# Kernel optimization log

Hardware: AMD Instinct MI355X
Metric: run time of the kernel (lower is better)

Reference implementation:

```python
import jax, jax.numpy as jnp
import numpy as np

D_MODEL = 768
D_STATE = 128
EXPAND = 2
D_CONV = 4
HEADDIM = 48
D_INNER = EXPAND * D_MODEL            # 1536
NHEADS = D_INNER // HEADDIM           # 32
CONV_DIM = D_INNER + 2 * D_STATE      # 1792 (ngroups=1)
D_IN_PROJ = 2 * D_INNER + 2 * D_STATE + NHEADS  # 3360
EPS = 1e-5


def setup_inputs() -> dict:
    key = jax.random.key(0)
    ks = jax.random.split(key, 8)
    B, L = 2, 1024
    x = jax.random.normal(ks[0], (B, L, D_MODEL), dtype=jnp.float32)
    in_proj_w = jax.random.normal(ks[1], (D_IN_PROJ, D_MODEL), dtype=jnp.float32) * 0.02
    conv_w = jax.random.normal(ks[2], (CONV_DIM, D_CONV), dtype=jnp.float32) * 0.1
    conv_b = jnp.zeros((CONV_DIM,), dtype=jnp.float32)
    # dt init as in Mamba2: dt ~ logspace[1e-3, 1e-1], dt_bias = softplus^-1(dt)
    u = jax.random.uniform(ks[3], (NHEADS,), dtype=jnp.float32)
    dt = jnp.exp(u * (np.log(0.1) - np.log(0.001)) + np.log(0.001))
    dt_bias = jnp.log(jnp.expm1(dt))
    # A in [1, 16]
    A_log = jnp.log(jax.random.uniform(ks[4], (NHEADS,), dtype=jnp.float32) * 15.0 + 1.0)
    D = jnp.ones((NHEADS,), dtype=jnp.float32)
    rms_w = jnp.ones((D_INNER,), dtype=jnp.float32)
    out_proj_w = jax.random.normal(ks[5], (D_MODEL, D_INNER), dtype=jnp.float32) * 0.02
    ln_w = jnp.ones((D_MODEL,), dtype=jnp.float32)
    ln_b = jnp.zeros((D_MODEL,), dtype=jnp.float32)
    return {"x": x, "in_proj_w": in_proj_w, "conv_w": conv_w, "conv_b": conv_b,
            "dt_bias": dt_bias, "A_log": A_log, "D": D, "rms_w": rms_w,
            "out_proj_w": out_proj_w, "ln_w": ln_w, "ln_b": ln_b}


def _mamba_block(x, in_proj_w, conv_w, conv_b, dt_bias, A_log, D, rms_w, out_proj_w, ln_w, ln_b):
    B, L, _ = x.shape
    zxbcdt = jnp.einsum('bld,ed->ble', x, in_proj_w)          # (B,L,D_IN_PROJ)
    z = zxbcdt[..., :D_INNER]                                  # gate
    xBC = zxbcdt[..., D_INNER:D_INNER + CONV_DIM]              # (B,L,CONV_DIM)
    dt = jax.nn.softplus(zxbcdt[..., -NHEADS:] + dt_bias)      # (B,L,H)

    # causal depthwise conv1d (kernel 4) + SiLU
    xp = jnp.pad(xBC, ((0, 0), (D_CONV - 1, 0), (0, 0)))
    conv = conv_b
    for k in range(D_CONV):
        conv = conv + xp[:, k:k + L, :] * conv_w[:, k]
    xBC = jax.nn.silu(conv)

    xs = xBC[..., :D_INNER].reshape(B, L, NHEADS, HEADDIM)     # (B,L,H,P)
    Bm = xBC[..., D_INNER:D_INNER + D_STATE]                   # (B,L,N)
    Cm = xBC[..., D_INNER + D_STATE:]                          # (B,L,N)

    A = -jnp.exp(A_log)                                        # (H,)
    dA = jnp.exp(dt * A)                                       # (B,L,H)
    xdt = xs * dt[..., None]                                   # (B,L,H,P)

    def step(h, inp):
        dA_t, xdt_t, B_t, C_t = inp                            # (B,H),(B,H,P),(B,N),(B,N)
        h = h * dA_t[:, :, None, None] + jnp.einsum('bhp,bn->bhpn', xdt_t, B_t)
        y_t = jnp.einsum('bhpn,bn->bhp', h, C_t)
        return h, y_t

    h0 = jnp.zeros((B, NHEADS, HEADDIM, D_STATE), dtype=x.dtype)
    _, ys = jax.lax.scan(step, h0,
                         (dA.transpose(1, 0, 2), xdt.transpose(1, 0, 2, 3),
                          Bm.transpose(1, 0, 2), Cm.transpose(1, 0, 2)))
    y = ys.transpose(1, 0, 2, 3) + D[None, None, :, None] * xs  # (B,L,H,P)
    y = y.reshape(B, L, D_INNER)

    # gated RMSNorm: rmsnorm(y * silu(z)) * rms_w
    yg = y * jax.nn.silu(z)
    yg = yg * jax.lax.rsqrt(jnp.mean(yg * yg, axis=-1, keepdims=True) + EPS) * rms_w
    out = jnp.einsum('ble,de->bld', yg, out_proj_w)

    # residual + LayerNorm
    r = out + x
    mu = jnp.mean(r, axis=-1, keepdims=True)
    var = jnp.mean((r - mu) ** 2, axis=-1, keepdims=True)
    return (r - mu) * jax.lax.rsqrt(var + EPS) * ln_w + ln_b


def reference(x, in_proj_w, conv_w, conv_b, dt_bias, A_log, D, rms_w, out_proj_w, ln_w, ln_b):
    return _mamba_block(x, in_proj_w, conv_w, conv_b, dt_bias, A_log, D, rms_w,
                        out_proj_w, ln_w, ln_b)
```

## Files before the change

kernel.cpp:

```cpp
#include <hip/hip_runtime.h>
#include <math.h>

#define BDIM 2
#define LLEN 1024
#define DMODEL 768
#define DINNER 1536
#define DSTATE 128
#define NH 32
#define HD 48
#define CONVD 1792
#define DPROJ 3360
#define DPROJP 3456
#define QCH 128
#define NCH 8
#define ROWS (BDIM*LLEN)

typedef unsigned short ushort_t;
typedef __attribute__((ext_vector_type(4))) short short4v;
typedef __attribute__((ext_vector_type(8))) short short8v;
typedef __attribute__((ext_vector_type(4))) float floatx4;

#define OFF_ZX   0ull
#define OFF_XBC  (OFF_ZX  + (size_t)ROWS*DPROJP)
#define OFF_DT   (OFF_XBC + (size_t)ROWS*CONVD)
#define OFF_LA   (OFF_DT  + (size_t)ROWS*NH)
#define OFF_SC   (OFF_LA  + (size_t)ROWS*NH)
#define OFF_Y    (OFF_SC  + (size_t)BDIM*NH*NCH*HD*DSTATE)
#define OFF_PP   (OFF_Y   + (size_t)ROWS*DINNER)
#define OFF_CBT  (OFF_PP  + 1024ull)
#define OFF_CBF  (OFF_CBT + 262144ull)
#define OFF_BBF  (OFF_CBF + 131072ull)
#define OFF_BTBF (OFF_BBF + 131072ull)
#define OFF_XPT  (OFF_BTBF+ 131072ull)

__device__ __forceinline__ ushort_t f2bf(float f) {
  union { float f; unsigned int u; } v; v.f = f;
  return (ushort_t)((v.u + 0x7FFFu + ((v.u >> 16) & 1u)) >> 16);
}
__device__ __forceinline__ float bf2f(short s) {
  union { unsigned int u; float f; } v; v.u = ((unsigned int)(ushort_t)s) << 16;
  return v.f;
}

#define GLOAD_LDS16(gptr, lptr) \
  __builtin_amdgcn_global_load_lds( \
      (const __attribute__((address_space(1))) void*)(gptr), \
      (__attribute__((address_space(3))) void*)(lptr), 16, 0, 0)

__global__ __launch_bounds__(256) void convert_bf16_kernel(
    const float* __restrict__ in, ushort_t* __restrict__ out, int n8) {
  const int i = blockIdx.x * 256 + threadIdx.x;
  if (i >= n8) return;
  const float4 a = ((const float4*)in)[i * 2];
  const float4 b = ((const float4*)in)[i * 2 + 1];
  short8v o;
  o[0] = (short)f2bf(a.x); o[1] = (short)f2bf(a.y);
  o[2] = (short)f2bf(a.z); o[3] = (short)f2bf(a.w);
  o[4] = (short)f2bf(b.x); o[5] = (short)f2bf(b.y);
  o[6] = (short)f2bf(b.z); o[7] = (short)f2bf(b.w);
  *(short8v*)(out + (size_t)i * 8) = o;
}

__global__ __launch_bounds__(256) void convert_wpad_kernel(
    const float* __restrict__ w, ushort_t* __restrict__ out) {
  const int i = blockIdx.x * 256 + threadIdx.x;
  if (i >= DPROJP * (DMODEL / 8)) return;
  const int row = i / (DMODEL / 8);
  short8v o;
  if (row < DPROJ) {
    const float4 a = ((const float4*)w)[i * 2];
    const float4 b = ((const float4*)w)[i * 2 + 1];
    o[0] = (short)f2bf(a.x); o[1] = (short)f2bf(a.y);
    o[2] = (short)f2bf(a.z); o[3] = (short)f2bf(a.w);
    o[4] = (short)f2bf(b.x); o[5] = (short)f2bf(b.y);
    o[6] = (short)f2bf(b.z); o[7] = (short)f2bf(b.w);
  } else {
    for (int j = 0; j < 8; j++) o[j] = 0;
  }
  *(short8v*)(out + (size_t)i * 8) = o;
}

__global__ __launch_bounds__(256) void gemm_bf16(
    const ushort_t* __restrict__ A, const ushort_t* __restrict__ B,
    float* __restrict__ C, int M, int N, int K) {
  __shared__ __align__(16) ushort_t As[128 * 32];
  __shared__ __align__(16) ushort_t Bs[128 * 32];
  const int tid = threadIdx.x;
  const int lane = tid & 63;
  const int w = tid >> 6;
  const int wm = (w >> 1) * 64, wn = (w & 1) * 64;
  const int m0 = blockIdx.y * 128, n0 = blockIdx.x * 128;

  floatx4 acc[4][4];
#pragma unroll
  for (int i = 0; i < 4; i++)
#pragma unroll
    for (int j = 0; j < 4; j++) acc[i][j] = (floatx4){0.f, 0.f, 0.f, 0.f};

  const int srow = tid >> 2;
  const int skc = (tid & 3) * 8;
  const int kk = (lane >> 4) * 8;
  const int fr = lane & 15;

  for (int k0 = 0; k0 < K; k0 += 32) {
#pragma unroll
    for (int i = 0; i < 2; i++) {
      GLOAD_LDS16(A + (size_t)(m0 + i * 64 + srow) * K + k0 + skc,
                  As + (i * 64 + srow) * 32 + skc);
      GLOAD_LDS16(B + (size_t)(n0 + i * 64 + srow) * K + k0 + skc,
                  Bs + (i * 64 + srow) * 32 + skc);
    }
    __syncthreads();
    short8v a[4], bv[4];
#pragma unroll
    for (int mr = 0; mr < 4; mr++)
      a[mr] = *(const short8v*)(As + (wm + mr * 16 + fr) * 32 + kk);
#pragma unroll
    for (int nc = 0; nc < 4; nc++)
      bv[nc] = *(const short8v*)(Bs + (wn + nc * 16 + fr) * 32 + kk);
#pragma unroll
    for (int mr = 0; mr < 4; mr++)
#pragma unroll
      for (int nc = 0; nc < 4; nc++)
        acc[mr][nc] = __builtin_amdgcn_mfma_f32_16x16x32_bf16(
            a[mr], bv[nc], acc[mr][nc], 0, 0, 0);
    __syncthreads();
  }

  const int crow = (lane >> 4) * 4;
#pragma unroll
  for (int mr = 0; mr < 4; mr++)
#pragma unroll
    for (int nc = 0; nc < 4; nc++)
#pragma unroll
      for (int j = 0; j < 4; j++)
        C[(size_t)(m0 + wm + mr * 16 + crow + j) * N + n0 + wn + nc * 16 + fr] =
            acc[mr][nc][j];
}

__global__ __launch_bounds__(256) void conv_dt_kernel(
    const float* __restrict__ zx, const float* __restrict__ conv_w,
    const float* __restrict__ conv_b, const float* __restrict__ dt_bias,
    float* __restrict__ xbc, float* __restrict__ dtbuf) {
  const int row = blockIdx.x;
  const int t = row % LLEN;
  const int tid = threadIdx.x;
  for (int c = tid; c < CONVD; c += 256) {
    float accv = conv_b[c];
#pragma unroll
    for (int k = 0; k < 4; k++) {
      const int tt = t - 3 + k;
      if (tt >= 0)
        accv += zx[(size_t)(row - 3 + k) * DPROJP + DINNER + c] * conv_w[c * 4 + k];
    }
    xbc[(size_t)row * CONVD + c] = accv / (1.f + expf(-accv));
  }
  if (tid < NH) {
    const float v = zx[(size_t)row * DPROJP + (DPROJ - NH) + tid] + dt_bias[tid];
    dtbuf[row * NH + tid] = (v > 20.f) ? v : log1pf(expf(v));
  }
}

__global__ __launch_bounds__(128) void cumsum_kernel(
    const float* __restrict__ dtb, const float* __restrict__ A_log,
    float* __restrict__ la2, float* __restrict__ Pp) {
  const int c = blockIdx.x, h = blockIdx.y, b = blockIdx.z;
  const int tid = threadIdx.x, lane = tid & 63;
  const int row = b * LLEN + c * QCH + tid;
  __shared__ float s0;
  float v = dtb[(size_t)row * NH + h];
#pragma unroll
  for (int off = 1; off < 64; off <<= 1) {
    const float u = __shfl_up(v, off, 64);
    if (lane >= off) v += u;
  }
  if (tid == 63) s0 = v;
  __syncthreads();
  if (tid >= 64) v += s0;
  const float la2v = -expf(A_log[h]) * v * 1.44269504088896f;
  la2[(size_t)row * NH + h] = la2v;
  if (tid == 127) Pp[(b * NH + h) * NCH + c] = exp2f(la2v);
}

__global__ __launch_bounds__(256) void prep_bc_kernel(
    const float* __restrict__ xbc, ushort_t* __restrict__ Bbf,
    ushort_t* __restrict__ BTbf, ushort_t* __restrict__ Cbf) {
  const int bc = blockIdx.x;
  const int b = bc / NCH, c = bc % NCH;
  const int row0 = b * LLEN + c * QCH;
  const int tid = threadIdx.x;
  __shared__ ushort_t lb[128][136];
  for (int idx = tid; idx < 128 * 32; idx += 256) {
    const int t = idx >> 5, f4 = (idx & 31) * 4;
    const float4 v = *(const float4*)&xbc[(size_t)(row0 + t) * CONVD + DINNER + f4];
    short4v o;
    o[0] = (short)f2bf(v.x); o[1] = (short)f2bf(v.y);
    o[2] = (short)f2bf(v.z); o[3] = (short)f2bf(v.w);
    *(short4v*)&Bbf[(size_t)(bc * 128 + t) * 128 + f4] = o;
    *(short4v*)&lb[t][f4] = o;
  }
  for (int idx = tid; idx < 128 * 32; idx += 256) {
    const int t = idx >> 5, f4 = (idx & 31) * 4;
    const float4 v = *(const float4*)&xbc[(size_t)(row0 + t) * CONVD + DINNER + DSTATE + f4];
    short4v o;
    o[0] = (short)f2bf(v.x); o[1] = (short)f2bf(v.y);
    o[2] = (short)f2bf(v.z); o[3] = (short)f2bf(v.w);
    *(short4v*)&Cbf[(size_t)(bc * 128 + t) * 128 + f4] = o;
  }
  __syncthreads();
  for (int idx = tid; idx < 128 * 16; idx += 256) {
    const int n = idx & 127, t0 = (idx >> 7) * 8;
    short8v o;
#pragma unroll
    for (int j = 0; j < 8; j++) o[j] = lb[t0 + j][n];
    *(short8v*)&BTbf[(size_t)(bc * 128 + n) * 128 + t0] = o;
  }
}

__global__ __launch_bounds__(256) void prep_x_kernel(
    const float* __restrict__ xbc, const float* __restrict__ dtb,
    ushort_t* __restrict__ XpT) {
  const int c = blockIdx.x, h = blockIdx.y, b = blockIdx.z;
  const int row0 = b * LLEN + c * QCH;
  const int tid = threadIdx.x;
  __shared__ ushort_t xl[128][56];
  __shared__ float dts[128];
  if (tid < 128) dts[tid] = dtb[(size_t)(row0 + tid) * NH + h];
  __syncthreads();
  for (int idx = tid; idx < 128 * 12; idx += 256) {
    const int r = idx / 12, f4 = (idx % 12) * 4;
    const float4 v = *(const float4*)&xbc[(size_t)(row0 + r) * CONVD + h * HD + f4];
    const float d = dts[r];
    short4v o;
    o[0] = (short)f2bf(v.x * d); o[1] = (short)f2bf(v.y * d);
    o[2] = (short)f2bf(v.z * d); o[3] = (short)f2bf(v.w * d);
    *(short4v*)&xl[r][f4] = o;
  }
  __syncthreads();
  const size_t base = ((size_t)(b * NCH + c) * NH + h) * HD * 128;
  for (int idx = tid; idx < 48 * 16; idx += 256) {
    const int p = idx % 48, t0 = (idx / 48) * 8;
    short8v o;
#pragma unroll
    for (int j = 0; j < 8; j++) o[j] = xl[t0 + j][p];
    *(short8v*)&XpT[base + (size_t)p * 128 + t0] = o;
  }
}

__global__ __launch_bounds__(256) void cbt_kernel(
    const ushort_t* __restrict__ Cbf, const ushort_t* __restrict__ Bbf,
    float* __restrict__ CBt) {
  const int bc = blockIdx.x;
  const int tid = threadIdx.x, lane = tid & 63, w = tid >> 6;
  const int wm = w * 32;
  const int fr = lane & 15, kk = (lane >> 4) * 8;
  floatx4 acc[2][8];
#pragma unroll
  for (int i = 0; i < 2; i++)
#pragma unroll
    for (int j = 0; j < 8; j++) acc[i][j] = (floatx4){0.f, 0.f, 0.f, 0.f};
  for (int ki = 0; ki < 4; ki++) {
    const int kg = ki * 32 + kk;
    short8v a[2], bv[8];
#pragma unroll
    for (int mt = 0; mt < 2; mt++)
      a[mt] = *(const short8v*)&Cbf[(size_t)(bc * 128 + wm + mt * 16 + fr) * 128 + kg];
#pragma unroll
    for (int nt = 0; nt < 8; nt++)
      bv[nt] = *(const short8v*)&Bbf[(size_t)(bc * 128 + nt * 16 + fr) * 128 + kg];
#pragma unroll
    for (int mt = 0; mt < 2; mt++)
#pragma unroll
      for (int nt = 0; nt < 8; nt++)
        acc[mt][nt] = __builtin_amdgcn_mfma_f32_16x16x32_bf16(
            a[mt], bv[nt], acc[mt][nt], 0, 0, 0);
  }
  const int crow = (lane >> 4) * 4;
#pragma unroll
  for (int mt = 0; mt < 2; mt++)
#pragma unroll
    for (int nt = 0; nt < 8; nt++)
#pragma unroll
      for (int j = 0; j < 4; j++)
        CBt[(size_t)(bc * 128 + wm + mt * 16 + crow + j) * 128 + nt * 16 + fr] =
            acc[mt][nt][j];
}

__global__ __launch_bounds__(256) void stateA_kernel(
    const ushort_t* __restrict__ XpT, const ushort_t* __restrict__ BTbf,
    const float* __restrict__ la2, float* __restrict__ Sc) {
  const int c = blockIdx.x, h = blockIdx.y, b = blockIdx.z;
  const int bc = b * NCH + c, bh = b * NH + h;
  const int row0 = b * LLEN + c * QCH;
  const int tid = threadIdx.x, lane = tid & 63, w = tid >> 6;
  __shared__ float ew[128];
  const float laL = la2[(size_t)(row0 + 127) * NH + h];
  if (tid < 128) ew[tid] = exp2f(laL - la2[(size_t)(row0 + tid) * NH + h]);
  __syncthreads();
  const int wn = w * 32;
  const int fr = lane & 15, kk = (lane >> 4) * 8;
  const size_t xbase = ((size_t)bc * NH + h) * HD * 128;
  floatx4 acc[3][2];
#pragma unroll
  for (int i = 0; i < 3; i++)
#pragma unroll
    for (int j = 0; j < 2; j++) acc[i][j] = (floatx4){0.f, 0.f, 0.f, 0.f};
  for (int ki = 0; ki < 4; ki++) {
    const int kg = ki * 32 + kk;
    short8v a[3], bv[2];
#pragma unroll
    for (int mt = 0; mt < 3; mt++) {
      const short8v raw = *(const short8v*)&XpT[xbase + (size_t)(mt * 16 + fr) * 128 + kg];
      short8v s;
#pragma unroll
      for (int e = 0; e < 8; e++) s[e] = (short)f2bf(bf2f(raw[e]) * ew[kg + e]);
      a[mt] = s;
    }
#pragma unroll
    for (int nt = 0; nt < 2; nt++)
      bv[nt] = *(const short8v*)&BTbf[(size_t)(bc * 128 + wn + nt * 16 + fr) * 128 + kg];
#pragma unroll
    for (int mt = 0; mt < 3; mt++)
#pragma unroll
      for (int nt = 0; nt < 2; nt++)
        acc[mt][nt] = __builtin_amdgcn_mfma_f32_16x16x32_bf16(
            a[mt], bv[nt], acc[mt][nt], 0, 0, 0);
  }
  const int crow = (lane >> 4) * 4;
  float* sc = Sc + (size_t)(bh * NCH + c) * (HD * DSTATE);
#pragma unroll
  for (int mt = 0; mt < 3; mt++)
#pragma unroll
    for (int nt = 0; nt < 2; nt++)
#pragma unroll
      for (int j = 0; j < 4; j++)
        sc[(size_t)(mt * 16 + crow + j) * 128 + wn + nt * 16 + fr] = acc[mt][nt][j];
}

__global__ __launch_bounds__(256) void chunk_combine_kernel(
    float* __restrict__ Sc, const float* __restrict__ Pp) {
  const int bh = blockIdx.x;
  const int tid = threadIdx.x;
  for (int e = tid; e < HD * DSTATE; e += 256) {
    float hv = 0.f;
#pragma unroll
    for (int c = 0; c < NCH; c++) {
      const size_t idx = ((size_t)(bh * NCH + c)) * HD * DSTATE + e;
      const float sv = Sc[idx];
      Sc[idx] = hv;
      hv = hv * Pp[bh * NCH + c] + sv;
    }
  }
}

__global__ __launch_bounds__(256) void ykernel(
    const float* __restrict__ CBt, const ushort_t* __restrict__ XpT,
    const ushort_t* __restrict__ Cbf, const float* __restrict__ Hc,
    const float* __restrict__ la2, float* __restrict__ y) {
  const int c = blockIdx.x, h = blockIdx.y, b = blockIdx.z;
  const int bc = b * NCH + c, bh = b * NH + h;
  const int row0 = b * LLEN + c * QCH;
  const int tid = threadIdx.x, lane = tid & 63, w = tid >> 6;
  __shared__ float laL[128], el[128];
  if (tid < 128) {
    const float v = la2[(size_t)(row0 + tid) * NH + h];
    laL[tid] = v; el[tid] = exp2f(v);
  }
  __syncthreads();
  const int wm = w * 32;
  const int fr = lane & 15, kk = (lane >> 4) * 8;
  const size_t xbase = ((size_t)bc * NH + h) * HD * 128;
  const float* hin = Hc + (size_t)(bh * NCH + c) * (HD * DSTATE);
  floatx4 acc[2][3];
#pragma unroll
  for (int i = 0; i < 2; i++)
#pragma unroll
    for (int j = 0; j < 3; j++) acc[i][j] = (floatx4){0.f, 0.f, 0.f, 0.f};

  for (int ki = 0; ki < 4; ki++) {
    const int kg = ki * 32 + kk;
    short8v a[2], bv[3];
#pragma unroll
    for (int mt = 0; mt < 2; mt++) {
      const int t = wm + mt * 16 + fr;
      const float lt = laL[t];
      const float* cb = &CBt[(size_t)(bc * 128 + t) * 128 + kg];
      const float4 u0 = *(const float4*)cb;
      const float4 u1 = *(const float4*)(cb + 4);
      const float f[8] = {u0.x, u0.y, u0.z, u0.w, u1.x, u1.y, u1.z, u1.w};
      short8v s;
#pragma unroll
      for (int e = 0; e < 8; e++) {
        const int sidx = kg + e;
        const float m = (t >= sidx) ? exp2f(lt - laL[sidx]) : 0.f;
        s[e] = (short)f2bf(f[e] * m);
      }
      a[mt] = s;
    }
#pragma unroll
    for (int nt = 0; nt < 3; nt++)
      bv[nt] = *(const short8v*)&XpT[xbase + (size_t)(nt * 16 + fr) * 128 + kg];
#pragma unroll
    for (int mt = 0; mt < 2; mt++)
#pragma unroll
      for (int nt = 0; nt < 3; nt++)
        acc[mt][nt] = __builtin_amdgcn_mfma_f32_16x16x32_bf16(
            a[mt], bv[nt], acc[mt][nt], 0, 0, 0);
  }
  for (int ki = 0; ki < 4; ki++) {
    const int kg = ki * 32 + kk;
    short8v a[2], bv[3];
#pragma unroll
    for (int mt = 0; mt < 2; mt++) {
      const int t = wm + mt * 16 + fr;
      const float scl = el[t];
      const short8v raw = *(const short8v*)&Cbf[(size_t)(bc * 128 + t) * 128 + kg];
      short8v s;
#pragma unroll
      for (int e = 0; e < 8; e++) s[e] = (short)f2bf(bf2f(raw[e]) * scl);
      a[mt] = s;
    }
#pragma unroll
    for (int nt = 0; nt < 3; nt++) {
      const float* hp = &hin[(size_t)(nt * 16 + fr) * 128 + kg];
      const float4 u0 = *(const float4*)hp;
      const float4 u1 = *(const float4*)(hp + 4);
      const float f[8] = {u0.x, u0.y, u0.z, u0.w, u1.x, u1.y, u1.z, u1.w};
      short8v s;
#pragma unroll
      for (int e = 0; e < 8; e++) s[e] = (short)f2bf(f[e]);
      bv[nt] = s;
    }
#pragma unroll
    for (int mt = 0; mt < 2; mt++)
#pragma unroll
      for (int nt = 0; nt < 3; nt++)
        acc[mt][nt] = __builtin_amdgcn_mfma_f32_16x16x32_bf16(
            a[mt], bv[nt], acc[mt][nt], 0, 0, 0);
  }
  const int crow = (lane >> 4) * 4;
#pragma unroll
  for (int mt = 0; mt < 2; mt++)
#pragma unroll
    for (int nt = 0; nt < 3; nt++)
#pragma unroll
      for (int j = 0; j < 4; j++) {
        const int row = row0 + wm + mt * 16 + crow + j;
        y[(size_t)row * DINNER + h * HD + nt * 16 + fr] = acc[mt][nt][j];
      }
}

__global__ __launch_bounds__(256) void gate_rms_kernel(
    const float* __restrict__ zx, const float* __restrict__ xbc,
    const float* __restrict__ Dv, const float* __restrict__ rms_w,
    const float* __restrict__ y, ushort_t* __restrict__ ybf) {
  const int row = blockIdx.x;
  const int tid = threadIdx.x;
  __shared__ float sred[4];
  float g[6];
  float ss = 0.f;
#pragma unroll
  for (int i = 0; i < 6; i++) {
    const int e = tid + i * 256;
    const float yv = y[(size_t)row * DINNER + e] + Dv[e / HD] * xbc[(size_t)row * CONVD + e];
    const float z = zx[(size_t)row * DPROJP + e];
    const float gv = yv * (z / (1.f + expf(-z)));
    g[i] = gv;
    ss += gv * gv;
  }
#pragma unroll
  for (int off = 32; off; off >>= 1) ss += __shfl_down(ss, off, 64);
  if ((tid & 63) == 0) sred[tid >> 6] = ss;
  __syncthreads();
  const float tot = sred[0] + sred[1] + sred[2] + sred[3];
  const float scale = rsqrtf(tot / DINNER + 1e-5f);
#pragma unroll
  for (int i = 0; i < 6; i++) {
    const int e = tid + i * 256;
    ybf[(size_t)row * DINNER + e] = f2bf(g[i] * scale * rms_w[e]);
  }
}

__global__ __launch_bounds__(256) void resid_ln_kernel(
    const float* __restrict__ go, const float* __restrict__ x,
    const float* __restrict__ ln_w, const float* __restrict__ ln_b,
    float* __restrict__ out) {
  const int row = blockIdx.x;
  const int tid = threadIdx.x;
  __shared__ float sred[4];
  __shared__ float sred2[4];
  float r[3];
  float s = 0.f;
#pragma unroll
  for (int i = 0; i < 3; i++) {
    const int e = tid + i * 256;
    r[i] = go[(size_t)row * DMODEL + e] + x[(size_t)row * DMODEL + e];
    s += r[i];
  }
#pragma unroll
  for (int off = 32; off; off >>= 1) s += __shfl_down(s, off, 64);
  if ((tid & 63) == 0) sred[tid >> 6] = s;
  __syncthreads();
  const float mu = (sred[0] + sred[1] + sred[2] + sred[3]) * (1.f / DMODEL);
  float s2 = 0.f;
#pragma unroll
  for (int i = 0; i < 3; i++) {
    const float d = r[i] - mu;
    s2 += d * d;
  }
#pragma unroll
  for (int off = 32; off; off >>= 1) s2 += __shfl_down(s2, off, 64);
  if ((tid & 63) == 0) sred2[tid >> 6] = s2;
  __syncthreads();
  const float var = (sred2[0] + sred2[1] + sred2[2] + sred2[3]) * (1.f / DMODEL);
  const float inv = rsqrtf(var + 1e-5f);
#pragma unroll
  for (int i = 0; i < 3; i++) {
    const int e = tid + i * 256;
    out[(size_t)row * DMODEL + e] = (r[i] - mu) * inv * ln_w[e] + ln_b[e];
  }
}

extern "C" void kernel_launch(void* const* d_in, const int* in_sizes, int n_in,
                              void* d_out, int out_size, void* d_ws, size_t ws_size,
                              hipStream_t stream) {
  const float* x          = (const float*)d_in[0];
  const float* in_proj_w  = (const float*)d_in[1];
  const float* conv_w     = (const float*)d_in[2];
  const float* conv_b     = (const float*)d_in[3];
  const float* dt_bias    = (const float*)d_in[4];
  const float* A_log      = (const float*)d_in[5];
  const float* Dv         = (const float*)d_in[6];
  const float* rms_w      = (const float*)d_in[7];
  const float* out_proj_w = (const float*)d_in[8];
  const float* ln_w       = (const float*)d_in[9];
  const float* ln_b       = (const float*)d_in[10];
  float* out = (float*)d_out;
  float* ws  = (float*)d_ws;

  float* zx   = ws + OFF_ZX;
  float* xbc  = ws + OFF_XBC;
  float* dtb  = ws + OFF_DT;
  float* la2  = ws + OFF_LA;
  float* Sc   = ws + OFF_SC;
  float* ybuf = ws + OFF_Y;
  float* Pp   = ws + OFF_PP;
  float* CBt  = ws + OFF_CBT;
  ushort_t* Cbf  = (ushort_t*)(ws + OFF_CBF);
  ushort_t* Bbf  = (ushort_t*)(ws + OFF_BBF);
  ushort_t* BTbf = (ushort_t*)(ws + OFF_BTBF);
  ushort_t* XpT  = (ushort_t*)(ws + OFF_XPT);

  ushort_t* xbf   = (ushort_t*)(ws + OFF_Y);
  ushort_t* ipwbf = (ushort_t*)(ws + OFF_Y + 786432);
  ushort_t* ybf   = (ushort_t*)(ws + OFF_SC);
  ushort_t* opwbf = (ushort_t*)(ws + OFF_SC + 1572864);
  float*    go    = ws + OFF_ZX;

  convert_bf16_kernel<<<(ROWS * DMODEL / 8 + 255) / 256, 256, 0, stream>>>(
      x, xbf, ROWS * DMODEL / 8);
  convert_wpad_kernel<<<(DPROJP * DMODEL / 8 + 255) / 256, 256, 0, stream>>>(
      in_proj_w, ipwbf);

  gemm_bf16<<<dim3(DPROJP / 128, ROWS / 128), 256, 0, stream>>>(
      xbf, ipwbf, zx, ROWS, DPROJP, DMODEL);

  conv_dt_kernel<<<ROWS, 256, 0, stream>>>(zx, conv_w, conv_b, dt_bias, xbc, dtb);

  cumsum_kernel<<<dim3(NCH, NH, BDIM), 128, 0, stream>>>(dtb, A_log, la2, Pp);
  prep_bc_kernel<<<BDIM * NCH, 256, 0, stream>>>(xbc, Bbf, BTbf, Cbf);
  prep_x_kernel<<<dim3(NCH, NH, BDIM), 256, 0, stream>>>(xbc, dtb, XpT);
  cbt_kernel<<<BDIM * NCH, 256, 0, stream>>>(Cbf, Bbf, CBt);
  stateA_kernel<<<dim3(NCH, NH, BDIM), 256, 0, stream>>>(XpT, BTbf, la2, Sc);
  chunk_combine_kernel<<<BDIM * NH, 256, 0, stream>>>(Sc, Pp);
  ykernel<<<dim3(NCH, NH, BDIM), 256, 0, stream>>>(CBt, XpT, Cbf, Sc, la2, ybuf);

  gate_rms_kernel<<<ROWS, 256, 0, stream>>>(zx, xbc, Dv, rms_w, ybuf, ybf);

  convert_bf16_kernel<<<(DMODEL * DINNER / 8 + 255) / 256, 256, 0, stream>>>(
      out_proj_w, opwbf, DMODEL * DINNER / 8);
  gemm_bf16<<<dim3(DMODEL / 128, ROWS / 128), 256, 0, stream>>>(
      ybf, opwbf, go, ROWS, DMODEL, DINNER);

  resid_ln_kernel<<<ROWS, 256, 0, stream>>>(go, x, ln_w, ln_b, out);
}
```

Baseline: 256.2 us.

## Store in-proj and conv outputs in bf16, fuse conversions, narrow out-proj tile

The in-projection GEMM now writes bf16 instead of fp32, and the conv kernel reads bf16, runs vectorized over four channels at a time, and writes xBC in bf16. The separate B/C bf16 copy buffers are dropped, so downstream kernels read directly from the bf16 xBC array. The two input conversion launches are merged into one kernel, gate_rms is vectorized to 8 elements per thread, and the out-projection GEMM uses 128x64 tiles to launch more blocks. The aim is to cut memory traffic and launch count, at the cost of extra bf16 rounding on z, dt and the conv output.

```diff
diff --git a/kernel.cpp b/kernel.cpp
--- a/kernel.cpp
+++ b/kernel.cpp
@@ -21,17 +21,15 @@
 typedef __attribute__((ext_vector_type(4))) float floatx4;
 
 #define OFF_ZX   0ull
-#define OFF_XBC  (OFF_ZX  + (size_t)ROWS*DPROJP)
-#define OFF_DT   (OFF_XBC + (size_t)ROWS*CONVD)
-#define OFF_LA   (OFF_DT  + (size_t)ROWS*NH)
-#define OFF_SC   (OFF_LA  + (size_t)ROWS*NH)
-#define OFF_Y    (OFF_SC  + (size_t)BDIM*NH*NCH*HD*DSTATE)
-#define OFF_PP   (OFF_Y   + (size_t)ROWS*DINNER)
-#define OFF_CBT  (OFF_PP  + 1024ull)
-#define OFF_CBF  (OFF_CBT + 262144ull)
-#define OFF_BBF  (OFF_CBF + 131072ull)
-#define OFF_BTBF (OFF_BBF + 131072ull)
-#define OFF_XPT  (OFF_BTBF+ 131072ull)
+#define OFF_XBC  3538944ull
+#define OFF_DT   5373952ull
+#define OFF_LA   5439488ull
+#define OFF_SC   5505024ull
+#define OFF_Y    8650752ull
+#define OFF_PP   11796480ull
+#define OFF_CBT  11797504ull
+#define OFF_BTBF 12059648ull
+#define OFF_XPT  12190720ull
 
 __device__ __forceinline__ ushort_t f2bf(float f) {
   union { float f; unsigned int u; } v; v.f = f;
@@ -46,6 +44,38 @@
   __builtin_amdgcn_global_load_lds( \
       (const __attribute__((address_space(1))) void*)(gptr), \
       (__attribute__((address_space(3))) void*)(lptr), 16, 0, 0)
+
+__global__ __launch_bounds__(256) void convert_in_kernel(
+    const float* __restrict__ x, const float* __restrict__ w,
+    ushort_t* __restrict__ xbf, ushort_t* __restrict__ ipwbf) {
+  const int blk = blockIdx.x;
+  if (blk < 768) {
+    const int i = blk * 256 + threadIdx.x;
+    const float4 a = ((const float4*)x)[i * 2];
+    const float4 b = ((const float4*)x)[i * 2 + 1];
+    short8v o;
+    o[0] = (short)f2bf(a.x); o[1] = (short)f2bf(a.y);
+    o[2] = (short)f2bf(a.z); o[3] = (short)f2bf(a.w);
+    o[4] = (short)f2bf(b.x); o[5] = (short)f2bf(b.y);
+    o[6] = (short)f2bf(b.z); o[7] = (short)f2bf(b.w);
+    *(short8v*)(xbf + (size_t)i * 8) = o;
+  } else {
+    const int i = (blk - 768) * 256 + threadIdx.x;
+    const int row = i / (DMODEL / 8);
+    short8v o;
+    if (row < DPROJ) {
+      const float4 a = ((const float4*)w)[i * 2];
+      const float4 b = ((const float4*)w)[i * 2 + 1];
+      o[0] = (short)f2bf(a.x); o[1] = (short)f2bf(a.y);
+      o[2] = (short)f2bf(a.z); o[3] = (short)f2bf(a.w);
+      o[4] = (short)f2bf(b.x); o[5] = (short)f2bf(b.y);
+      o[6] = (short)f2bf(b.z); o[7] = (short)f2bf(b.w);
+    } else {
+      for (int j = 0; j < 8; j++) o[j] = 0;
+    }
+    *(short8v*)(ipwbf + (size_t)i * 8) = o;
+  }
+}
 
 __global__ __launch_bounds__(256) void convert_bf16_kernel(
     const float* __restrict__ in, ushort_t* __restrict__ out, int n8) {
@@ -61,47 +91,21 @@
   *(short8v*)(out + (size_t)i * 8) = o;
 }
 
-__global__ __launch_bounds__(256) void convert_wpad_kernel(
-    const float* __restrict__ w, ushort_t* __restrict__ out) {
-  const int i = blockIdx.x * 256 + threadIdx.x;
-  if (i >= DPROJP * (DMODEL / 8)) return;
-  const int row = i / (DMODEL / 8);
-  short8v o;
-  if (row < DPROJ) {
-    const float4 a = ((const float4*)w)[i * 2];
-    const float4 b = ((const float4*)w)[i * 2 + 1];
-    o[0] = (short)f2bf(a.x); o[1] = (short)f2bf(a.y);
-    o[2] = (short)f2bf(a.z); o[3] = (short)f2bf(a.w);
-    o[4] = (short)f2bf(b.x); o[5] = (short)f2bf(b.y);
-    o[6] = (short)f2bf(b.z); o[7] = (short)f2bf(b.w);
-  } else {
-    for (int j = 0; j < 8; j++) o[j] = 0;
-  }
-  *(short8v*)(out + (size_t)i * 8) = o;
-}
-
-__global__ __launch_bounds__(256) void gemm_bf16(
+__global__ __launch_bounds__(256) void gemm_bf16_bfout(
     const ushort_t* __restrict__ A, const ushort_t* __restrict__ B,
-    float* __restrict__ C, int M, int N, int K) {
+    ushort_t* __restrict__ C, int M, int N, int K) {
   __shared__ __align__(16) ushort_t As[128 * 32];
   __shared__ __align__(16) ushort_t Bs[128 * 32];
-  const int tid = threadIdx.x;
-  const int lane = tid & 63;
-  const int w = tid >> 6;
+  const int tid = threadIdx.x, lane = tid & 63, w = tid >> 6;
   const int wm = (w >> 1) * 64, wn = (w & 1) * 64;
   const int m0 = blockIdx.y * 128, n0 = blockIdx.x * 128;
-
   floatx4 acc[4][4];
 #pragma unroll
   for (int i = 0; i < 4; i++)
 #pragma unroll
     for (int j = 0; j < 4; j++) acc[i][j] = (floatx4){0.f, 0.f, 0.f, 0.f};
-
-  const int srow = tid >> 2;
-  const int skc = (tid & 3) * 8;
-  const int kk = (lane >> 4) * 8;
-  const int fr = lane & 15;
-
+  const int srow = tid >> 2, skc = (tid & 3) * 8;
+  const int kk = (lane >> 4) * 8, fr = lane & 15;
   for (int k0 = 0; k0 < K; k0 += 32) {
 #pragma unroll
     for (int i = 0; i < 2; i++) {
@@ -126,12 +130,59 @@
             a[mr], bv[nc], acc[mr][nc], 0, 0, 0);
     __syncthreads();
   }
-
   const int crow = (lane >> 4) * 4;
 #pragma unroll
   for (int mr = 0; mr < 4; mr++)
 #pragma unroll
     for (int nc = 0; nc < 4; nc++)
+#pragma unroll
+      for (int j = 0; j < 4; j++)
+        C[(size_t)(m0 + wm + mr * 16 + crow + j) * N + n0 + wn + nc * 16 + fr] =
+            f2bf(acc[mr][nc][j]);
+}
+
+__global__ __launch_bounds__(256) void gemm_bf16_n64(
+    const ushort_t* __restrict__ A, const ushort_t* __restrict__ B,
+    float* __restrict__ C, int M, int N, int K) {
+  __shared__ __align__(16) ushort_t As[128 * 32];
+  __shared__ __align__(16) ushort_t Bs[64 * 32];
+  const int tid = threadIdx.x, lane = tid & 63, w = tid >> 6;
+  const int wm = (w >> 1) * 64, wn = (w & 1) * 32;
+  const int m0 = blockIdx.y * 128, n0 = blockIdx.x * 64;
+  floatx4 acc[4][2];
+#pragma unroll
+  for (int i = 0; i < 4; i++)
+#pragma unroll
+    for (int j = 0; j < 2; j++) acc[i][j] = (floatx4){0.f, 0.f, 0.f, 0.f};
+  const int srow = tid >> 2, skc = (tid & 3) * 8;
+  const int kk = (lane >> 4) * 8, fr = lane & 15;
+  for (int k0 = 0; k0 < K; k0 += 32) {
+#pragma unroll
+    for (int i = 0; i < 2; i++)
+      GLOAD_LDS16(A + (size_t)(m0 + i * 64 + srow) * K + k0 + skc,
+                  As + (i * 64 + srow) * 32 + skc);
+    GLOAD_LDS16(B + (size_t)(n0 + srow) * K + k0 + skc, Bs + srow * 32 + skc);
+    __syncthreads();
+    short8v a[4], bv[2];
+#pragma unroll
+    for (int mr = 0; mr < 4; mr++)
+      a[mr] = *(const short8v*)(As + (wm + mr * 16 + fr) * 32 + kk);
+#pragma unroll
+    for (int nc = 0; nc < 2; nc++)
+      bv[nc] = *(const short8v*)(Bs + (wn + nc * 16 + fr) * 32 + kk);
+#pragma unroll
+    for (int mr = 0; mr < 4; mr++)
+#pragma unroll
+      for (int nc = 0; nc < 2; nc++)
+        acc[mr][nc] = __builtin_amdgcn_mfma_f32_16x16x32_bf16(
+            a[mr], bv[nc], acc[mr][nc], 0, 0, 0);
+    __syncthreads();
+  }
+  const int crow = (lane >> 4) * 4;
+#pragma unroll
+  for (int mr = 0; mr < 4; mr++)
+#pragma unroll
+    for (int nc = 0; nc < 2; nc++)
 #pragma unroll
       for (int j = 0; j < 4; j++)
         C[(size_t)(m0 + wm + mr * 16 + crow + j) * N + n0 + wn + nc * 16 + fr] =
@@ -139,24 +190,38 @@
 }
 
 __global__ __launch_bounds__(256) void conv_dt_kernel(
-    const float* __restrict__ zx, const float* __restrict__ conv_w,
+    const ushort_t* __restrict__ zxb, const float* __restrict__ conv_w,
     const float* __restrict__ conv_b, const float* __restrict__ dt_bias,
-    float* __restrict__ xbc, float* __restrict__ dtbuf) {
+    ushort_t* __restrict__ xbcb, float* __restrict__ dtbuf) {
   const int row = blockIdx.x;
   const int t = row % LLEN;
   const int tid = threadIdx.x;
-  for (int c = tid; c < CONVD; c += 256) {
-    float accv = conv_b[c];
+  for (int g = tid; g < CONVD / 4; g += 256) {
+    const int c = g * 4;
+    const float4 cb = *(const float4*)&conv_b[c];
+    float acc0 = cb.x, acc1 = cb.y, acc2 = cb.z, acc3 = cb.w;
+    float4 cw[4];
+#pragma unroll
+    for (int j = 0; j < 4; j++) cw[j] = *(const float4*)&conv_w[(c + j) * 4];
 #pragma unroll
     for (int k = 0; k < 4; k++) {
-      const int tt = t - 3 + k;
-      if (tt >= 0)
-        accv += zx[(size_t)(row - 3 + k) * DPROJP + DINNER + c] * conv_w[c * 4 + k];
-    }
-    xbc[(size_t)row * CONVD + c] = accv / (1.f + expf(-accv));
+      if (t - 3 + k >= 0) {
+        const short4v v = *(const short4v*)&zxb[(size_t)(row - 3 + k) * DPROJP + DINNER + c];
+        acc0 += bf2f(v[0]) * ((const float*)&cw[0])[k];
+        acc1 += bf2f(v[1]) * ((const float*)&cw[1])[k];
+        acc2 += bf2f(v[2]) * ((const float*)&cw[2])[k];
+        acc3 += bf2f(v[3]) * ((const float*)&cw[3])[k];
+      }
+    }
+    short4v o;
+    o[0] = (short)f2bf(acc0 / (1.f + expf(-acc0)));
+    o[1] = (short)f2bf(acc1 / (1.f + expf(-acc1)));
+    o[2] = (short)f2bf(acc2 / (1.f + expf(-acc2)));
+    o[3] = (short)f2bf(acc3 / (1.f + expf(-acc3)));
+    *(short4v*)&xbcb[(size_t)row * CONVD + c] = o;
   }
   if (tid < NH) {
-    const float v = zx[(size_t)row * DPROJP + (DPROJ - NH) + tid] + dt_bias[tid];
+    const float v = bf2f(zxb[(size_t)row * DPROJP + (DPROJ - NH) + tid]) + dt_bias[tid];
     dtbuf[row * NH + tid] = (v > 20.f) ? v : log1pf(expf(v));
   }
 }
@@ -182,9 +247,8 @@
   if (tid == 127) Pp[(b * NH + h) * NCH + c] = exp2f(la2v);
 }
 
-__global__ __launch_bounds__(256) void prep_bc_kernel(
-    const float* __restrict__ xbc, ushort_t* __restrict__ Bbf,
-    ushort_t* __restrict__ BTbf, ushort_t* __restrict__ Cbf) {
+__global__ __launch_bounds__(256) void prep_bt_kernel(
+    const ushort_t* __restrict__ xbcb, ushort_t* __restrict__ BTbf) {
   const int bc = blockIdx.x;
   const int b = bc / NCH, c = bc % NCH;
   const int row0 = b * LLEN + c * QCH;
@@ -192,20 +256,8 @@
   __shared__ ushort_t lb[128][136];
   for (int idx = tid; idx < 128 * 32; idx += 256) {
     const int t = idx >> 5, f4 = (idx & 31) * 4;
-    const float4 v = *(const float4*)&xbc[(size_t)(row0 + t) * CONVD + DINNER + f4];
-    short4v o;
-    o[0] = (short)f2bf(v.x); o[1] = (short)f2bf(v.y);
-    o[2] = (short)f2bf(v.z); o[3] = (short)f2bf(v.w);
-    *(short4v*)&Bbf[(size_t)(bc * 128 + t) * 128 + f4] = o;
-    *(short4v*)&lb[t][f4] = o;
-  }
-  for (int idx = tid; idx < 128 * 32; idx += 256) {
-    const int t = idx >> 5, f4 = (idx & 31) * 4;
-    const float4 v = *(const float4*)&xbc[(size_t)(row0 + t) * CONVD + DINNER + DSTATE + f4];
-    short4v o;
-    o[0] = (short)f2bf(v.x); o[1] = (short)f2bf(v.y);
-    o[2] = (short)f2bf(v.z); o[3] = (short)f2bf(v.w);
-    *(short4v*)&Cbf[(size_t)(bc * 128 + t) * 128 + f4] = o;
+    const short4v v = *(const short4v*)&xbcb[(size_t)(row0 + t) * CONVD + DINNER + f4];
+    *(short4v*)&lb[t][f4] = v;
   }
   __syncthreads();
   for (int idx = tid; idx < 128 * 16; idx += 256) {
@@ -218,7 +270,7 @@
 }
 
 __global__ __launch_bounds__(256) void prep_x_kernel(
-    const float* __restrict__ xbc, const float* __restrict__ dtb,
+    const ushort_t* __restrict__ xbcb, const float* __restrict__ dtb,
     ushort_t* __restrict__ XpT) {
   const int c = blockIdx.x, h = blockIdx.y, b = blockIdx.z;
   const int row0 = b * LLEN + c * QCH;
@@ -229,11 +281,11 @@
   __syncthreads();
   for (int idx = tid; idx < 128 * 12; idx += 256) {
     const int r = idx / 12, f4 = (idx % 12) * 4;
-    const float4 v = *(const float4*)&xbc[(size_t)(row0 + r) * CONVD + h * HD + f4];
+    const short4v v = *(const short4v*)&xbcb[(size_t)(row0 + r) * CONVD + h * HD + f4];
     const float d = dts[r];
     short4v o;
-    o[0] = (short)f2bf(v.x * d); o[1] = (short)f2bf(v.y * d);
-    o[2] = (short)f2bf(v.z * d); o[3] = (short)f2bf(v.w * d);
+    o[0] = (short)f2bf(bf2f(v[0]) * d); o[1] = (short)f2bf(bf2f(v[1]) * d);
+    o[2] = (short)f2bf(bf2f(v[2]) * d); o[3] = (short)f2bf(bf2f(v[3]) * d);
     *(short4v*)&xl[r][f4] = o;
   }
   __syncthreads();
@@ -248,9 +300,10 @@
 }
 
 __global__ __launch_bounds__(256) void cbt_kernel(
-    const ushort_t* __restrict__ Cbf, const ushort_t* __restrict__ Bbf,
-    float* __restrict__ CBt) {
+    const ushort_t* __restrict__ xbcb, float* __restrict__ CBt) {
   const int bc = blockIdx.x;
+  const int b = bc / NCH, c = bc % NCH;
+  const int row0 = b * LLEN + c * QCH;
   const int tid = threadIdx.x, lane = tid & 63, w = tid >> 6;
   const int wm = w * 32;
   const int fr = lane & 15, kk = (lane >> 4) * 8;
@@ -264,10 +317,12 @@
     short8v a[2], bv[8];
 #pragma unroll
     for (int mt = 0; mt < 2; mt++)
-      a[mt] = *(const short8v*)&Cbf[(size_t)(bc * 128 + wm + mt * 16 + fr) * 128 + kg];
+      a[mt] = *(const short8v*)&xbcb[(size_t)(row0 + wm + mt * 16 + fr) * CONVD +
+                                     DINNER + DSTATE + kg];
 #pragma unroll
     for (int nt = 0; nt < 8; nt++)
-      bv[nt] = *(const short8v*)&Bbf[(size_t)(bc * 128 + nt * 16 + fr) * 128 + kg];
+      bv[nt] = *(const short8v*)&xbcb[(size_t)(row0 + nt * 16 + fr) * CONVD +
+                                      DINNER + kg];
 #pragma unroll
     for (int mt = 0; mt < 2; mt++)
 #pragma unroll
@@ -355,7 +410,7 @@
 
 __global__ __launch_bounds__(256) void ykernel(
     const float* __restrict__ CBt, const ushort_t* __restrict__ XpT,
-    const ushort_t* __restrict__ Cbf, const float* __restrict__ Hc,
+    const ushort_t* __restrict__ xbcb, const float* __restrict__ Hc,
     const float* __restrict__ la2, float* __restrict__ y) {
   const int c = blockIdx.x, h = blockIdx.y, b = blockIdx.z;
   const int bc = b * NCH + c, bh = b * NH + h;
@@ -414,7 +469,8 @@
     for (int mt = 0; mt < 2; mt++) {
       const int t = wm + mt * 16 + fr;
       const float scl = el[t];
-      const short8v raw = *(const short8v*)&Cbf[(size_t)(bc * 128 + t) * 128 + kg];
+      const short8v raw = *(const short8v*)&xbcb[(size_t)(row0 + t) * CONVD +
+                                                 DINNER + DSTATE + kg];
       short8v s;
 #pragma unroll
       for (int e = 0; e < 8; e++) s[e] = (short)f2bf(bf2f(raw[e]) * scl);
@@ -451,22 +507,33 @@
 }
 
 __global__ __launch_bounds__(256) void gate_rms_kernel(
-    const float* __restrict__ zx, const float* __restrict__ xbc,
+    const ushort_t* __restrict__ zxb, const ushort_t* __restrict__ xbcb,
     const float* __restrict__ Dv, const float* __restrict__ rms_w,
     const float* __restrict__ y, ushort_t* __restrict__ ybf) {
   const int row = blockIdx.x;
   const int tid = threadIdx.x;
   __shared__ float sred[4];
-  float g[6];
+  float g[8];
   float ss = 0.f;
-#pragma unroll
-  for (int i = 0; i < 6; i++) {
-    const int e = tid + i * 256;
-    const float yv = y[(size_t)row * DINNER + e] + Dv[e / HD] * xbc[(size_t)row * CONVD + e];
-    const float z = zx[(size_t)row * DPROJP + e];
-    const float gv = yv * (z / (1.f + expf(-z)));
-    g[i] = gv;
-    ss += gv * gv;
+  if (tid < 192) {
+    const int e0 = tid * 8;
+    const short8v xv = *(const short8v*)&xbcb[(size_t)row * CONVD + e0];
+    const short8v zv = *(const short8v*)&zxb[(size_t)row * DPROJP + e0];
+    const float4 y0 = *(const float4*)&y[(size_t)row * DINNER + e0];
+    const float4 y1 = *(const float4*)&y[(size_t)row * DINNER + e0 + 4];
+    const float yf[8] = {y0.x, y0.y, y0.z, y0.w, y1.x, y1.y, y1.z, y1.w};
+#pragma unroll
+    for (int j = 0; j < 8; j++) {
+      const int e = e0 + j;
+      const float yv = yf[j] + Dv[e / HD] * bf2f(xv[j]);
+      const float z = bf2f(zv[j]);
+      const float gv = yv * (z / (1.f + expf(-z)));
+      g[j] = gv;
+      ss += gv * gv;
+    }
+  } else {
+#pragma unroll
+    for (int j = 0; j < 8; j++) g[j] = 0.f;
   }
 #pragma unroll
   for (int off = 32; off; off >>= 1) ss += __shfl_down(ss, off, 64);
@@ -474,10 +541,15 @@
   __syncthreads();
   const float tot = sred[0] + sred[1] + sred[2] + sred[3];
   const float scale = rsqrtf(tot / DINNER + 1e-5f);
-#pragma unroll
-  for (int i = 0; i < 6; i++) {
-    const int e = tid + i * 256;
-    ybf[(size_t)row * DINNER + e] = f2bf(g[i] * scale * rms_w[e]);
+  if (tid < 192) {
+    const int e0 = tid * 8;
+    const float4 w0 = *(const float4*)&rms_w[e0];
+    const float4 w1 = *(const float4*)&rms_w[e0 + 4];
+    const float wf[8] = {w0.x, w0.y, w0.z, w0.w, w1.x, w1.y, w1.z, w1.w};
+    short8v o;
+#pragma unroll
+    for (int j = 0; j < 8; j++) o[j] = (short)f2bf(g[j] * scale * wf[j]);
+    *(short8v*)&ybf[(size_t)row * DINNER + e0] = o;
   }
 }
 
@@ -538,16 +610,14 @@
   float* out = (float*)d_out;
   float* ws  = (float*)d_ws;
 
-  float* zx   = ws + OFF_ZX;
-  float* xbc  = ws + OFF_XBC;
+  ushort_t* zxb  = (ushort_t*)(ws + OFF_ZX);
+  ushort_t* xbcb = (ushort_t*)(ws + OFF_XBC);
   float* dtb  = ws + OFF_DT;
   float* la2  = ws + OFF_LA;
   float* Sc   = ws + OFF_SC;
   float* ybuf = ws + OFF_Y;
   float* Pp   = ws + OFF_PP;
   float* CBt  = ws + OFF_CBT;
-  ushort_t* Cbf  = (ushort_t*)(ws + OFF_CBF);
-  ushort_t* Bbf  = (ushort_t*)(ws + OFF_BBF);
   ushort_t* BTbf = (ushort_t*)(ws + OFF_BTBF);
   ushort_t* XpT  = (ushort_t*)(ws + OFF_XPT);
 
@@ -557,29 +627,26 @@
   ushort_t* opwbf = (ushort_t*)(ws + OFF_SC + 1572864);
   float*    go    = ws + OFF_ZX;
 
-  convert_bf16_kernel<<<(ROWS * DMODEL / 8 + 255) / 256, 256, 0, stream>>>(
-      x, xbf, ROWS * DMODEL / 8);
-  convert_wpad_kernel<<<(DPROJP * DMODEL / 8 + 255) / 256, 256, 0, stream>>>(
-      in_proj_w, ipwbf);
-
-  gemm_bf16<<<dim3(DPROJP / 128, ROWS / 128), 256, 0, stream>>>(
-      xbf, ipwbf, zx, ROWS, DPROJP, DMODEL);
-
-  conv_dt_kernel<<<ROWS, 256, 0, stream>>>(zx, conv_w, conv_b, dt_bias, xbc, dtb);
+  convert_in_kernel<<<2064, 256, 0, stream>>>(x, in_proj_w, xbf, ipwbf);
+
+  gemm_bf16_bfout<<<dim3(DPROJP / 128, ROWS / 128), 256, 0, stream>>>(
+      xbf, ipwbf, zxb, ROWS, DPROJP, DMODEL);
+
+  conv_dt_kernel<<<ROWS, 256, 0, stream>>>(zxb, conv_w, conv_b, dt_bias, xbcb, dtb);
 
   cumsum_kernel<<<dim3(NCH, NH, BDIM), 128, 0, stream>>>(dtb, A_log, la2, Pp);
-  prep_bc_kernel<<<BDIM * NCH, 256, 0, stream>>>(xbc, Bbf, BTbf, Cbf);
-  prep_x_kernel<<<dim3(NCH, NH, BDIM), 256, 0, stream>>>(xbc, dtb, XpT);
-  cbt_kernel<<<BDIM * NCH, 256, 0, stream>>>(Cbf, Bbf, CBt);
+  prep_bt_kernel<<<BDIM * NCH, 256, 0, stream>>>(xbcb, BTbf);
+  prep_x_kernel<<<dim3(NCH, NH, BDIM), 256, 0, stream>>>(xbcb, dtb, XpT);
+  cbt_kernel<<<BDIM * NCH, 256, 0, stream>>>(xbcb, CBt);
   stateA_kernel<<<dim3(NCH, NH, BDIM), 256, 0, stream>>>(XpT, BTbf, la2, Sc);
   chunk_combine_kernel<<<BDIM * NH, 256, 0, stream>>>(Sc, Pp);
-  ykernel<<<dim3(NCH, NH, BDIM), 256, 0, stream>>>(CBt, XpT, Cbf, Sc, la2, ybuf);
-
-  gate_rms_kernel<<<ROWS, 256, 0, stream>>>(zx, xbc, Dv, rms_w, ybuf, ybf);
+  ykernel<<<dim3(NCH, NH, BDIM), 256, 0, stream>>>(CBt, XpT, xbcb, Sc, la2, ybuf);
+
+  gate_rms_kernel<<<ROWS, 256, 0, stream>>>(zxb, xbcb, Dv, rms_w, ybuf, ybf);
 
   convert_bf16_kernel<<<(DMODEL * DINNER / 8 + 255) / 256, 256, 0, stream>>>(
       out_proj_w, opwbf, DMODEL * DINNER / 8);
-  gemm_bf16<<<dim3(DMODEL / 128, ROWS / 128), 256, 0, stream>>>(
+  gemm_bf16_n64<<<dim3(DMODEL / 64, ROWS / 128), 256, 0, stream>>>(
       ybf, opwbf, go, ROWS, DMODEL, DINNER);
 
   resid_ln_kernel<<<ROWS, 256, 0, stream>>>(go, x, ln_w, ln_b, out);
```

New measurement: 234.4 us. 8.5% less time.
